# Kernel tuning notes

Measured on AMD Instinct MI355X. Metric: run time of the kernel, lower is better.

## Reference

```python
import jax, jax.numpy as jnp
import numpy as np

VOCAB = 32000
DIM = 1024
SEQ = 4096


def setup_inputs() -> dict:
    key = jax.random.key(0)
    ks = jax.random.split(key, 6)
    x = jax.random.randint(ks[0], (1, SEQ), 0, VOCAB, dtype=jnp.int64 if jax.config.jax_enable_x64 else jnp.int32)
    emb = jax.random.normal(ks[1], (VOCAB, DIM), dtype=jnp.float32) * 0.02
    norm_w = jnp.ones((DIM,), dtype=jnp.float32)
    Wq = jax.random.normal(ks[2], (DIM, DIM), dtype=jnp.float32) * (1.0 / np.sqrt(DIM))
    Wk = jax.random.normal(ks[3], (DIM, DIM), dtype=jnp.float32) * (1.0 / np.sqrt(DIM))
    Wv = jax.random.normal(ks[4], (DIM, DIM), dtype=jnp.float32) * (1.0 / np.sqrt(DIM))
    return {"x": x, "emb": emb, "norm_w": norm_w, "Wq": Wq, "Wk": Wk, "Wv": Wv}


def reference(x, emb, norm_w, Wq, Wk, Wv):
    # embedding lookup: [1, S, D]
    h = emb[x]
    # RMSNorm (torch nn.RMSNorm with eps=None -> finfo(dtype).eps)
    eps = jnp.finfo(h.dtype).eps
    h = h * jax.lax.rsqrt(jnp.mean(h * h, axis=-1, keepdims=True) + eps) * norm_w
    h = h[0]  # squeeze(0) -> [S, D]
    # QKV projections (torch Linear: y = x @ W.T)
    q = h @ Wq.T
    k = h @ Wk.T
    v = h @ Wv.T
    # NOTE: faithful to source -- no 1/sqrt(d) scaling, no causal mask
    attn = jax.nn.softmax(q @ k.T, axis=-1)  # [S, S]
    out = attn @ v  # [S, D]
    return jax.nn.silu(out)
```

## Files before the change

### kernel.cpp

```cpp
#include <hip/hip_runtime.h>
#include <stdint.h>

#define SEQ 4096
#define DIM 1024

typedef __bf16 bf16x8 __attribute__((ext_vector_type(8)));
typedef float f32x4 __attribute__((ext_vector_type(4)));
typedef unsigned short u16;

__device__ __forceinline__ u16 f2bf(float f) {
    unsigned u = __float_as_uint(f);
    u += 0x7fffu + ((u >> 16) & 1u);
    return (u16)(u >> 16);
}
__device__ __forceinline__ float bf2f(u16 h) {
    return __uint_as_float(((unsigned)h) << 16);
}

__device__ __forceinline__ void gload16(const u16* g, u16* l) {
    __builtin_amdgcn_global_load_lds(
        (const __attribute__((address_space(1))) void*)g,
        (__attribute__((address_space(3))) void*)l, 16, 0, 0);
}

__global__ __launch_bounds__(256) void embed_rmsnorm_split(
    const int* __restrict__ x, const float* __restrict__ emb,
    const float* __restrict__ nw, u16* __restrict__ hhl)
{
    const int row  = blockIdx.x;
    const int t    = threadIdx.x;
    const int lane = t & 63, wave = t >> 6;

    bool i64 = true;
    #pragma unroll
    for (int i = 1; i < 128; i += 2) i64 = i64 && (x[i] == 0);
    const int id = i64 ? x[2 * row] : x[row];

    float4 e = *(const float4*)(emb + (size_t)id * DIM + t * 4);
    float ss = e.x*e.x + e.y*e.y + e.z*e.z + e.w*e.w;
    #pragma unroll
    for (int off = 32; off > 0; off >>= 1) ss += __shfl_down(ss, off);

    __shared__ float red[4];
    if (lane == 0) red[wave] = ss;
    __syncthreads();
    float sum = red[0] + red[1] + red[2] + red[3];
    float scale = rsqrtf(sum * (1.0f / DIM) + 1.1920929e-7f);

    float4 n = *(const float4*)(nw + t * 4);
    float o0 = e.x * scale * n.x;
    float o1 = e.y * scale * n.y;
    float o2 = e.z * scale * n.z;
    float o3 = e.w * scale * n.w;
    ushort4 oh, ol;
    u16 b;
    b = f2bf(o0); oh.x = b; ol.x = f2bf(o0 - bf2f(b));
    b = f2bf(o1); oh.y = b; ol.y = f2bf(o1 - bf2f(b));
    b = f2bf(o2); oh.z = b; ol.z = f2bf(o2 - bf2f(b));
    b = f2bf(o3); oh.w = b; ol.w = f2bf(o3 - bf2f(b));
    *(ushort4*)(hhl + (size_t)row * 2048 + t * 4)        = oh;
    *(ushort4*)(hhl + (size_t)row * 2048 + t * 4 + 1024) = ol;
}

__global__ __launch_bounds__(256) void split_w(
    const float* __restrict__ W0, const float* __restrict__ W1,
    const float* __restrict__ W2, u16* __restrict__ Whl)
{
    const float* W = (blockIdx.y == 0) ? W0 : (blockIdx.y == 1) ? W1 : W2;
    const int i   = (blockIdx.x * 256 + threadIdx.x) * 4;
    const int row = i >> 10;
    const int col = i & 1023;
    float4 w = *(const float4*)(W + i);
    ushort4 h, l;
    u16 b;
    b = f2bf(w.x); h.x = b; l.x = f2bf(w.x - bf2f(b));
    b = f2bf(w.y); h.y = b; l.y = f2bf(w.y - bf2f(b));
    b = f2bf(w.z); h.z = b; l.z = f2bf(w.z - bf2f(b));
    b = f2bf(w.w); h.w = b; l.w = f2bf(w.w - bf2f(b));
    u16* d = Whl + (size_t)(blockIdx.y * 1024 + row) * 2048 + col;
    *(ushort4*)(d)        = h;
    *(ushort4*)(d + 1024) = l;
}

#define NT32 32
template<int EPI>
__global__ __launch_bounds__(512, 2) void gemm_bk32(
    const u16* __restrict__ A, const u16* __restrict__ B,
    float* __restrict__ C,
    u16* __restrict__ O0, u16* __restrict__ O1, u16* __restrict__ OT)
{
    __shared__ __align__(16) u16 AhL[2][8192];
    __shared__ __align__(16) u16 AlL[2][8192];
    __shared__ __align__(16) u16 BhL[2][8192];
    __shared__ __align__(16) u16 BlL[2][8192];

    const int tid  = threadIdx.x;
    const int lane = tid & 63;
    const int wid  = tid >> 6;
    const int wm   = wid >> 2;
    const int wn   = wid & 3;
    const int l16  = lane & 15;
    const int half = lane >> 4;

    const int nx  = gridDim.x;
    const int nwg = nx * gridDim.y;
    const int wg  = blockIdx.y * nx + blockIdx.x;
    const int swz = (wg & 7) * (nwg >> 3) + (wg >> 3);
    const int m0  = (swz / nx) * 256;
    const int n0  = (swz % nx) * 256;

    const int srow = tid >> 2;
    const int scol = ((tid & 3) ^ ((tid >> 3) & 3)) * 8;
    const int ldst = tid * 8;
    const u16* pAh[2]; const u16* pAl[2]; const u16* pBh[2]; const u16* pBl[2];
    #pragma unroll
    for (int u = 0; u < 2; ++u) {
        const size_t ao = (size_t)(m0 + u * 128 + srow) * 2048 + scol;
        const size_t bo = (size_t)(n0 + u * 128 + srow) * 2048 + scol;
        pAh[u] = A + ao;  pAl[u] = A + ao + 1024;
        pBh[u] = B + bo;  pBl[u] = B + bo + 1024;
    }

    #pragma unroll
    for (int kk = 0; kk < 2; ++kk)
        #pragma unroll
        for (int u = 0; u < 2; ++u) {
            gload16(pAh[u] + kk * 32, &AhL[kk][u * 4096 + ldst]);
            gload16(pAl[u] + kk * 32, &AlL[kk][u * 4096 + ldst]);
            gload16(pBh[u] + kk * 32, &BhL[kk][u * 4096 + ldst]);
            gload16(pBl[u] + kk * 32, &BlL[kk][u * 4096 + ldst]);
        }
    asm volatile("s_waitcnt vmcnt(8)" ::: "memory");
    __builtin_amdgcn_sched_barrier(0);
    __builtin_amdgcn_s_barrier();

    f32x4 acc[8][4] = {};
    const int rc = 8 * (half ^ ((l16 >> 1) & 3));
    const int ab = (wm * 128 + l16) * 32 + rc;
    const int bb = (wn * 64  + l16) * 32 + rc;

    bf16x8 ah[4], al[4], bh[4], bl[4];

    #pragma unroll 1
    for (int t = 0; t < NT32; ++t) {
        const int  b  = t & 1;
        const bool ds = (t + 2) < NT32;
        const int  k2 = (t + 2) * 32;

        #pragma unroll
        for (int i = 0; i < 4; ++i) {
            ah[i] = *(const bf16x8*)&AhL[b][ab + i * 512];
            al[i] = *(const bf16x8*)&AlL[b][ab + i * 512];
        }
        #pragma unroll
        for (int g = 0; g < 2; ++g) {
            bh[g] = *(const bf16x8*)&BhL[b][bb + g * 512];
            bl[g] = *(const bf16x8*)&BlL[b][bb + g * 512];
        }
        __builtin_amdgcn_s_barrier();
        asm volatile("s_waitcnt lgkmcnt(0)" ::: "memory");
        __builtin_amdgcn_sched_barrier(0);
        __builtin_amdgcn_s_setprio(1);
        #pragma unroll
        for (int i = 0; i < 4; ++i)
            #pragma unroll
            for (int g = 0; g < 2; ++g) {
                acc[i][g] = __builtin_amdgcn_mfma_f32_16x16x32_bf16(ah[i], bh[g], acc[i][g], 0, 0, 0);
                acc[i][g] = __builtin_amdgcn_mfma_f32_16x16x32_bf16(ah[i], bl[g], acc[i][g], 0, 0, 0);
                acc[i][g] = __builtin_amdgcn_mfma_f32_16x16x32_bf16(al[i], bh[g], acc[i][g], 0, 0, 0);
            }
        __builtin_amdgcn_s_setprio(0);
        __builtin_amdgcn_s_barrier();

        #pragma unroll
        for (int g = 0; g < 2; ++g) {
            bh[2 + g] = *(const bf16x8*)&BhL[b][bb + (2 + g) * 512];
            bl[2 + g] = *(const bf16x8*)&BlL[b][bb + (2 + g) * 512];
        }
        __builtin_amdgcn_s_barrier();
        asm volatile("s_waitcnt lgkmcnt(0)" ::: "memory");
        __builtin_amdgcn_sched_barrier(0);
        __builtin_amdgcn_s_setprio(1);
        #pragma unroll
        for (int i = 0; i < 4; ++i)
            #pragma unroll
            for (int g = 0; g < 2; ++g) {
                acc[i][2 + g] = __builtin_amdgcn_mfma_f32_16x16x32_bf16(ah[i], bh[2 + g], acc[i][2 + g], 0, 0, 0);
                acc[i][2 + g] = __builtin_amdgcn_mfma_f32_16x16x32_bf16(ah[i], bl[2 + g], acc[i][2 + g], 0, 0, 0);
                acc[i][2 + g] = __builtin_amdgcn_mfma_f32_16x16x32_bf16(al[i], bh[2 + g], acc[i][2 + g], 0, 0, 0);
            }
        __builtin_amdgcn_s_setprio(0);
        __builtin_amdgcn_s_barrier();

        #pragma unroll
        for (int i = 0; i < 4; ++i) {
            ah[i] = *(const bf16x8*)&AhL[b][ab + 2048 + i * 512];
            al[i] = *(const bf16x8*)&AlL[b][ab + 2048 + i * 512];
        }
        if (ds) {
            gload16(pBh[0] + k2, &BhL[b][ldst]);
            gload16(pBh[1] + k2, &BhL[b][4096 + ldst]);
            gload16(pBl[0] + k2, &BlL[b][ldst]);
            gload16(pBl[1] + k2, &BlL[b][4096 + ldst]);
        }
        __builtin_amdgcn_s_barrier();
        asm volatile("s_waitcnt lgkmcnt(0)" ::: "memory");
        __builtin_amdgcn_sched_barrier(0);
        __builtin_amdgcn_s_setprio(1);
        #pragma unroll
        for (int i = 0; i < 4; ++i)
            #pragma unroll
            for (int g = 0; g < 2; ++g) {
                acc[4 + i][2 + g] = __builtin_amdgcn_mfma_f32_16x16x32_bf16(ah[i], bh[2 + g], acc[4 + i][2 + g], 0, 0, 0);
                acc[4 + i][2 + g] = __builtin_amdgcn_mfma_f32_16x16x32_bf16(ah[i], bl[2 + g], acc[4 + i][2 + g], 0, 0, 0);
                acc[4 + i][2 + g] = __builtin_amdgcn_mfma_f32_16x16x32_bf16(al[i], bh[2 + g], acc[4 + i][2 + g], 0, 0, 0);
            }
        __builtin_amdgcn_s_setprio(0);
        __builtin_amdgcn_s_barrier();

        if (ds) {
            gload16(pAh[0] + k2, &AhL[b][ldst]);
            gload16(pAh[1] + k2, &AhL[b][4096 + ldst]);
            gload16(pAl[0] + k2, &AlL[b][ldst]);
            gload16(pAl[1] + k2, &AlL[b][4096 + ldst]);
        }
        __builtin_amdgcn_s_barrier();
        __builtin_amdgcn_s_setprio(1);
        #pragma unroll
        for (int i = 0; i < 4; ++i)
            #pragma unroll
            for (int g = 0; g < 2; ++g) {
                acc[4 + i][g] = __builtin_amdgcn_mfma_f32_16x16x32_bf16(ah[i], bh[g], acc[4 + i][g], 0, 0, 0);
                acc[4 + i][g] = __builtin_amdgcn_mfma_f32_16x16x32_bf16(ah[i], bl[g], acc[4 + i][g], 0, 0, 0);
                acc[4 + i][g] = __builtin_amdgcn_mfma_f32_16x16x32_bf16(al[i], bh[g], acc[4 + i][g], 0, 0, 0);
            }
        __builtin_amdgcn_s_setprio(0);
        if (t < NT32 - 2) { asm volatile("s_waitcnt vmcnt(8)" ::: "memory"); }
        else              { asm volatile("s_waitcnt vmcnt(0)" ::: "memory"); }
        __builtin_amdgcn_sched_barrier(0);
        __builtin_amdgcn_s_barrier();
    }

    const int crow0 = m0 + wm * 128 + half * 4;
    const int ccol0 = n0 + wn * 64 + l16;
    if constexpr (EPI == 0) {
        #pragma unroll
        for (int mf = 0; mf < 8; ++mf)
            #pragma unroll
            for (int nf = 0; nf < 4; ++nf)
                #pragma unroll
                for (int r = 0; r < 4; ++r)
                    C[(size_t)(crow0 + mf * 16 + r) * SEQ + ccol0 + nf * 16] = acc[mf][nf][r];
    } else {
        const int reg = n0 >> 10;
        #pragma unroll
        for (int mf = 0; mf < 8; ++mf)
            #pragma unroll
            for (int nf = 0; nf < 4; ++nf)
                #pragma unroll
                for (int r = 0; r < 4; ++r) {
                    const int row = crow0 + mf * 16 + r;
                    const int c   = (ccol0 + nf * 16) & 1023;
                    const float val = acc[mf][nf][r];
                    const u16 hi = f2bf(val);
                    if (reg == 0) {
                        O0[(size_t)row * 2048 + c]        = hi;
                        O0[(size_t)row * 2048 + c + 1024] = f2bf(val - bf2f(hi));
                    } else if (reg == 1) {
                        O1[(size_t)row * 2048 + c]        = hi;
                        O1[(size_t)row * 2048 + c + 1024] = f2bf(val - bf2f(hi));
                    } else {
                        OT[(size_t)c * SEQ + row] = hi;
                    }
                }
    }
}

__global__ __launch_bounds__(256) void softmax_rows(float* __restrict__ S)
{
    const int row  = blockIdx.x;
    const int t    = threadIdx.x;
    const int lane = t & 63, wave = t >> 6;
    float* rp = S + (size_t)row * SEQ;

    float v[16];
    #pragma unroll
    for (int i = 0; i < 4; ++i) {
        float4 f = *(const float4*)(rp + i * 1024 + t * 4);
        v[i*4+0] = f.x; v[i*4+1] = f.y; v[i*4+2] = f.z; v[i*4+3] = f.w;
    }

    float m = v[0];
    #pragma unroll
    for (int i = 1; i < 16; ++i) m = fmaxf(m, v[i]);
    #pragma unroll
    for (int off = 32; off > 0; off >>= 1) m = fmaxf(m, __shfl_down(m, off));
    __shared__ float red[4];
    if (lane == 0) red[wave] = m;
    __syncthreads();
    m = fmaxf(fmaxf(red[0], red[1]), fmaxf(red[2], red[3]));
    __syncthreads();

    float s = 0.0f;
    #pragma unroll
    for (int i = 0; i < 16; ++i) { v[i] = __expf(v[i] - m); s += v[i]; }
    #pragma unroll
    for (int off = 32; off > 0; off >>= 1) s += __shfl_down(s, off);
    if (lane == 0) red[wave] = s;
    __syncthreads();
    s = red[0] + red[1] + red[2] + red[3];
    float inv = 1.0f / s;

    u16* op = (u16*)rp;
    #pragma unroll
    for (int i = 0; i < 4; ++i) {
        ushort4 o;
        o.x = f2bf(v[i*4+0] * inv);
        o.y = f2bf(v[i*4+1] * inv);
        o.z = f2bf(v[i*4+2] * inv);
        o.w = f2bf(v[i*4+3] * inv);
        *(ushort4*)(op + i * 1024 + t * 4) = o;
    }
}

__global__ __launch_bounds__(256, 3) void gemm_pv_partial(
    const u16* __restrict__ A, const u16* __restrict__ B,
    float* __restrict__ P0, float* __restrict__ P1)
{
    __shared__ __align__(16) u16 As[128 * 32];
    __shared__ __align__(16) u16 Bs[128 * 32];

    const int tid  = threadIdx.x;
    const int lane = tid & 63;
    const int wave = tid >> 6;
    const int m0   = blockIdx.y * 128;
    const int n0   = blockIdx.x * 128;
    const int wr   = (wave >> 1) * 64;
    const int wc   = (wave & 1) * 64;
    const int half = lane >> 4;
    const int l16  = lane & 15;

    float* C = blockIdx.z ? P1 : P0;
    const int kbase = blockIdx.z * 2048;

    f32x4 acc[4][4] = {};
    const int arow = tid >> 2;
    const int acol = (tid & 3) * 8;
    const int wb   = wave * 512;

    for (int k0 = kbase; k0 < kbase + 2048; k0 += 32) {
        __syncthreads();
        gload16(A + (size_t)(m0 + arow)      * 8192 + k0 + acol, &As[wb]);
        gload16(A + (size_t)(m0 + 64 + arow) * 8192 + k0 + acol, &As[2048 + wb]);
        gload16(B + (size_t)(n0 + arow)      * 4096 + k0 + acol, &Bs[wb]);
        gload16(B + (size_t)(n0 + 64 + arow) * 4096 + k0 + acol, &Bs[2048 + wb]);
        __syncthreads();

        bf16x8 af[4], bfr[4];
        #pragma unroll
        for (int i = 0; i < 4; ++i)
            af[i] = *(const bf16x8*)&As[(wr + i*16 + l16) * 32 + half * 8];
        #pragma unroll
        for (int j = 0; j < 4; ++j)
            bfr[j] = *(const bf16x8*)&Bs[(wc + j*16 + l16) * 32 + half * 8];
        #pragma unroll
        for (int i = 0; i < 4; ++i)
            #pragma unroll
            for (int j = 0; j < 4; ++j)
                acc[i][j] = __builtin_amdgcn_mfma_f32_16x16x32_bf16(af[i], bfr[j], acc[i][j], 0, 0, 0);
    }

    #pragma unroll
    for (int i = 0; i < 4; ++i)
        #pragma unroll
        for (int j = 0; j < 4; ++j)
            #pragma unroll
            for (int r = 0; r < 4; ++r) {
                int row = m0 + wr + i * 16 + half * 4 + r;
                int col = n0 + wc + j * 16 + l16;
                C[(size_t)row * DIM + col] = acc[i][j][r];
            }
}

__global__ __launch_bounds__(256) void combine_silu(
    const float* __restrict__ P0, const float* __restrict__ P1,
    float* __restrict__ out)
{
    const int i = (blockIdx.x * 256 + threadIdx.x) * 4;
    float4 a = *(const float4*)(P0 + i);
    float4 b = *(const float4*)(P1 + i);
    float4 o;
    float v;
    v = a.x + b.x; o.x = v / (1.0f + __expf(-v));
    v = a.y + b.y; o.y = v / (1.0f + __expf(-v));
    v = a.z + b.z; o.z = v / (1.0f + __expf(-v));
    v = a.w + b.w; o.w = v / (1.0f + __expf(-v));
    *(float4*)(out + i) = o;
}

extern "C" void kernel_launch(void* const* d_in, const int* in_sizes, int n_in,
                              void* d_out, int out_size, void* d_ws, size_t ws_size,
                              hipStream_t stream)
{
    const int*   x   = (const int*)d_in[0];
    const float* emb = (const float*)d_in[1];
    const float* nw  = (const float*)d_in[2];
    const float* Wq  = (const float*)d_in[3];
    const float* Wk  = (const float*)d_in[4];
    const float* Wv  = (const float*)d_in[5];
    float* out = (float*)d_out;

    char* ws = (char*)d_ws;
    u16*   vT  = (u16*)(ws);
    u16*   qhl = (u16*)(ws + ( 8u << 20));
    u16*   khl = (u16*)(ws + (24u << 20));
    float* Sc  = (float*)(ws + (40u << 20));
    u16*   hhl = (u16*)(ws + (40u << 20));
    u16*   Whl = (u16*)(ws + (56u << 20));
    float* P0  = (float*)(ws + ( 8u << 20));
    float* P1  = (float*)(ws + (24u << 20));

    embed_rmsnorm_split<<<SEQ, 256, 0, stream>>>(x, emb, nw, hhl);
    split_w<<<dim3(DIM * DIM / 1024, 3), 256, 0, stream>>>(Wq, Wk, Wv, Whl);

    gemm_bk32<1><<<dim3(3072 / 256, SEQ / 256), 512, 0, stream>>>(
        hhl, Whl, nullptr, qhl, khl, vT);

    gemm_bk32<0><<<dim3(SEQ / 256, SEQ / 256), 512, 0, stream>>>(
        qhl, khl, Sc, nullptr, nullptr, nullptr);

    softmax_rows<<<SEQ, 256, 0, stream>>>(Sc);

    gemm_pv_partial<<<dim3(DIM / 128, SEQ / 128, 2), 256, 0, stream>>>(
        (const u16*)Sc, vT, P0, P1);

    combine_silu<<<SEQ * DIM / 1024, 256, 0, stream>>>(P0, P1, out);
}
```

Before: 452.6 us.

## Retile QKV GEMM to 192-wide N tiles and split PV K four ways

The QKV projection GEMM is templated on N-fragment count so it runs with 256x192 tiles (16x16 grid = 256 workgroups) instead of 256x256 (12x16 = 192), aiming for better CU fill. The PV GEMM splits K into four 1024-long chunks instead of two, doubling workgroups. The extra partial sums are written into the unused upper columns of the score buffer, and the combine kernel sums four partials before SiLU. This adds more partial-sum traffic and relies on Sc bf16 data living only in the lower half of each row.

```diff
diff --git a/kernel.cpp b/kernel.cpp
--- a/kernel.cpp
+++ b/kernel.cpp
@@ -83,16 +83,17 @@
 }
 
 #define NT32 32
-template<int EPI>
+template<int EPI, int NF>
 __global__ __launch_bounds__(512, 2) void gemm_bk32(
     const u16* __restrict__ A, const u16* __restrict__ B,
     float* __restrict__ C,
     u16* __restrict__ O0, u16* __restrict__ O1, u16* __restrict__ OT)
 {
+    constexpr int BN = NF * 64;
     __shared__ __align__(16) u16 AhL[2][8192];
     __shared__ __align__(16) u16 AlL[2][8192];
-    __shared__ __align__(16) u16 BhL[2][8192];
-    __shared__ __align__(16) u16 BlL[2][8192];
+    __shared__ __align__(16) u16 BhL[2][NF * 2048];
+    __shared__ __align__(16) u16 BlL[2][NF * 2048];
 
     const int tid  = threadIdx.x;
     const int lane = tid & 63;
@@ -107,39 +108,47 @@
     const int wg  = blockIdx.y * nx + blockIdx.x;
     const int swz = (wg & 7) * (nwg >> 3) + (wg >> 3);
     const int m0  = (swz / nx) * 256;
-    const int n0  = (swz % nx) * 256;
+    const int n0  = (swz % nx) * BN;
 
     const int srow = tid >> 2;
     const int scol = ((tid & 3) ^ ((tid >> 3) & 3)) * 8;
     const int ldst = tid * 8;
-    const u16* pAh[2]; const u16* pAl[2]; const u16* pBh[2]; const u16* pBl[2];
-    #pragma unroll
-    for (int u = 0; u < 2; ++u) {
-        const size_t ao = (size_t)(m0 + u * 128 + srow) * 2048 + scol;
-        const size_t bo = (size_t)(n0 + u * 128 + srow) * 2048 + scol;
-        pAh[u] = A + ao;  pAl[u] = A + ao + 1024;
-        pBh[u] = B + bo;  pBl[u] = B + bo + 1024;
-    }
-
-    #pragma unroll
-    for (int kk = 0; kk < 2; ++kk)
-        #pragma unroll
-        for (int u = 0; u < 2; ++u) {
-            gload16(pAh[u] + kk * 32, &AhL[kk][u * 4096 + ldst]);
-            gload16(pAl[u] + kk * 32, &AlL[kk][u * 4096 + ldst]);
-            gload16(pBh[u] + kk * 32, &BhL[kk][u * 4096 + ldst]);
-            gload16(pBl[u] + kk * 32, &BlL[kk][u * 4096 + ldst]);
-        }
-    asm volatile("s_waitcnt vmcnt(8)" ::: "memory");
+    const u16* pAh0 = A + (size_t)(m0 + srow) * 2048 + scol;
+    const u16* pAh1 = A + (size_t)(m0 + 128 + srow) * 2048 + scol;
+    const u16* pAl0 = pAh0 + 1024;
+    const u16* pAl1 = pAh1 + 1024;
+    const u16* pBh0 = B + (size_t)(n0 + srow) * 2048 + scol;
+    const u16* pBl0 = pBh0 + 1024;
+    const u16* pBh1 = (NF == 4) ? B + (size_t)(n0 + 128 + srow) * 2048 + scol
+                                : B + (size_t)(n0 +  64 + srow) * 2048 + scol;
+    const u16* pBl1 = pBh1 + 1024;
+    const int  bdst1 = (NF == 4) ? 4096 + ldst : 2048 + ldst;
+    const bool doB1  = (NF == 4) || (wid >= 4);
+
+    #pragma unroll
+    for (int kk = 0; kk < 2; ++kk) {
+        gload16(pAh0 + kk * 32, &AhL[kk][ldst]);
+        gload16(pAh1 + kk * 32, &AhL[kk][4096 + ldst]);
+        gload16(pAl0 + kk * 32, &AlL[kk][ldst]);
+        gload16(pAl1 + kk * 32, &AlL[kk][4096 + ldst]);
+        gload16(pBh0 + kk * 32, &BhL[kk][ldst]);
+        gload16(pBl0 + kk * 32, &BlL[kk][ldst]);
+        if (doB1) {
+            gload16(pBh1 + kk * 32, &BhL[kk][bdst1]);
+            gload16(pBl1 + kk * 32, &BlL[kk][bdst1]);
+        }
+    }
+    if (NF == 4 || wid >= 4) { asm volatile("s_waitcnt vmcnt(8)" ::: "memory"); }
+    else                     { asm volatile("s_waitcnt vmcnt(6)" ::: "memory"); }
     __builtin_amdgcn_sched_barrier(0);
     __builtin_amdgcn_s_barrier();
 
-    f32x4 acc[8][4] = {};
+    f32x4 acc[8][NF] = {};
     const int rc = 8 * (half ^ ((l16 >> 1) & 3));
     const int ab = (wm * 128 + l16) * 32 + rc;
-    const int bb = (wn * 64  + l16) * 32 + rc;
-
-    bf16x8 ah[4], al[4], bh[4], bl[4];
+    const int bb = (wn * (NF * 16) + l16) * 32 + rc;
+
+    bf16x8 ah[4], al[4], bh[NF], bl[NF];
 
     #pragma unroll 1
     for (int t = 0; t < NT32; ++t) {
@@ -173,9 +182,9 @@
         __builtin_amdgcn_s_barrier();
 
         #pragma unroll
-        for (int g = 0; g < 2; ++g) {
-            bh[2 + g] = *(const bf16x8*)&BhL[b][bb + (2 + g) * 512];
-            bl[2 + g] = *(const bf16x8*)&BlL[b][bb + (2 + g) * 512];
+        for (int g = 2; g < NF; ++g) {
+            bh[g] = *(const bf16x8*)&BhL[b][bb + g * 512];
+            bl[g] = *(const bf16x8*)&BlL[b][bb + g * 512];
         }
         __builtin_amdgcn_s_barrier();
         asm volatile("s_waitcnt lgkmcnt(0)" ::: "memory");
@@ -184,10 +193,10 @@
         #pragma unroll
         for (int i = 0; i < 4; ++i)
             #pragma unroll
-            for (int g = 0; g < 2; ++g) {
-                acc[i][2 + g] = __builtin_amdgcn_mfma_f32_16x16x32_bf16(ah[i], bh[2 + g], acc[i][2 + g], 0, 0, 0);
-                acc[i][2 + g] = __builtin_amdgcn_mfma_f32_16x16x32_bf16(ah[i], bl[2 + g], acc[i][2 + g], 0, 0, 0);
-                acc[i][2 + g] = __builtin_amdgcn_mfma_f32_16x16x32_bf16(al[i], bh[2 + g], acc[i][2 + g], 0, 0, 0);
+            for (int g = 2; g < NF; ++g) {
+                acc[i][g] = __builtin_amdgcn_mfma_f32_16x16x32_bf16(ah[i], bh[g], acc[i][g], 0, 0, 0);
+                acc[i][g] = __builtin_amdgcn_mfma_f32_16x16x32_bf16(ah[i], bl[g], acc[i][g], 0, 0, 0);
+                acc[i][g] = __builtin_amdgcn_mfma_f32_16x16x32_bf16(al[i], bh[g], acc[i][g], 0, 0, 0);
             }
         __builtin_amdgcn_s_setprio(0);
         __builtin_amdgcn_s_barrier();
@@ -198,10 +207,12 @@
             al[i] = *(const bf16x8*)&AlL[b][ab + 2048 + i * 512];
         }
         if (ds) {
-            gload16(pBh[0] + k2, &BhL[b][ldst]);
-            gload16(pBh[1] + k2, &BhL[b][4096 + ldst]);
-            gload16(pBl[0] + k2, &BlL[b][ldst]);
-            gload16(pBl[1] + k2, &BlL[b][4096 + ldst]);
+            gload16(pBh0 + k2, &BhL[b][ldst]);
+            gload16(pBl0 + k2, &BlL[b][ldst]);
+            if (doB1) {
+                gload16(pBh1 + k2, &BhL[b][bdst1]);
+                gload16(pBl1 + k2, &BlL[b][bdst1]);
+            }
         }
         __builtin_amdgcn_s_barrier();
         asm volatile("s_waitcnt lgkmcnt(0)" ::: "memory");
@@ -210,19 +221,19 @@
         #pragma unroll
         for (int i = 0; i < 4; ++i)
             #pragma unroll
-            for (int g = 0; g < 2; ++g) {
-                acc[4 + i][2 + g] = __builtin_amdgcn_mfma_f32_16x16x32_bf16(ah[i], bh[2 + g], acc[4 + i][2 + g], 0, 0, 0);
-                acc[4 + i][2 + g] = __builtin_amdgcn_mfma_f32_16x16x32_bf16(ah[i], bl[2 + g], acc[4 + i][2 + g], 0, 0, 0);
-                acc[4 + i][2 + g] = __builtin_amdgcn_mfma_f32_16x16x32_bf16(al[i], bh[2 + g], acc[4 + i][2 + g], 0, 0, 0);
+            for (int g = 2; g < NF; ++g) {
+                acc[4 + i][g] = __builtin_amdgcn_mfma_f32_16x16x32_bf16(ah[i], bh[g], acc[4 + i][g], 0, 0, 0);
+                acc[4 + i][g] = __builtin_amdgcn_mfma_f32_16x16x32_bf16(ah[i], bl[g], acc[4 + i][g], 0, 0, 0);
+                acc[4 + i][g] = __builtin_amdgcn_mfma_f32_16x16x32_bf16(al[i], bh[g], acc[4 + i][g], 0, 0, 0);
             }
         __builtin_amdgcn_s_setprio(0);
         __builtin_amdgcn_s_barrier();
 
         if (ds) {
-            gload16(pAh[0] + k2, &AhL[b][ldst]);
-            gload16(pAh[1] + k2, &AhL[b][4096 + ldst]);
-            gload16(pAl[0] + k2, &AlL[b][ldst]);
-            gload16(pAl[1] + k2, &AlL[b][4096 + ldst]);
+            gload16(pAh0 + k2, &AhL[b][ldst]);
+            gload16(pAh1 + k2, &AhL[b][4096 + ldst]);
+            gload16(pAl0 + k2, &AlL[b][ldst]);
+            gload16(pAl1 + k2, &AlL[b][4096 + ldst]);
         }
         __builtin_amdgcn_s_barrier();
         __builtin_amdgcn_s_setprio(1);
@@ -235,32 +246,37 @@
                 acc[4 + i][g] = __builtin_amdgcn_mfma_f32_16x16x32_bf16(al[i], bh[g], acc[4 + i][g], 0, 0, 0);
             }
         __builtin_amdgcn_s_setprio(0);
-        if (t < NT32 - 2) { asm volatile("s_waitcnt vmcnt(8)" ::: "memory"); }
-        else              { asm volatile("s_waitcnt vmcnt(0)" ::: "memory"); }
+        if (t < NT32 - 2) {
+            if (NF == 4 || wid >= 4) { asm volatile("s_waitcnt vmcnt(8)" ::: "memory"); }
+            else                     { asm volatile("s_waitcnt vmcnt(6)" ::: "memory"); }
+        } else {
+            asm volatile("s_waitcnt vmcnt(0)" ::: "memory");
+        }
         __builtin_amdgcn_sched_barrier(0);
         __builtin_amdgcn_s_barrier();
     }
 
     const int crow0 = m0 + wm * 128 + half * 4;
-    const int ccol0 = n0 + wn * 64 + l16;
+    const int wcol  = n0 + wn * (NF * 16);
     if constexpr (EPI == 0) {
         #pragma unroll
         for (int mf = 0; mf < 8; ++mf)
             #pragma unroll
-            for (int nf = 0; nf < 4; ++nf)
+            for (int nf = 0; nf < NF; ++nf)
                 #pragma unroll
                 for (int r = 0; r < 4; ++r)
-                    C[(size_t)(crow0 + mf * 16 + r) * SEQ + ccol0 + nf * 16] = acc[mf][nf][r];
+                    C[(size_t)(crow0 + mf * 16 + r) * SEQ + wcol + nf * 16 + l16] = acc[mf][nf][r];
     } else {
-        const int reg = n0 >> 10;
-        #pragma unroll
-        for (int mf = 0; mf < 8; ++mf)
-            #pragma unroll
-            for (int nf = 0; nf < 4; ++nf)
+        #pragma unroll
+        for (int nf = 0; nf < NF; ++nf) {
+            const int base = wcol + nf * 16;
+            const int reg  = base >> 10;
+            const int c    = (base & 1023) + l16;
+            #pragma unroll
+            for (int mf = 0; mf < 8; ++mf)
                 #pragma unroll
                 for (int r = 0; r < 4; ++r) {
                     const int row = crow0 + mf * 16 + r;
-                    const int c   = (ccol0 + nf * 16) & 1023;
                     const float val = acc[mf][nf][r];
                     const u16 hi = f2bf(val);
                     if (reg == 0) {
@@ -273,6 +289,7 @@
                         OT[(size_t)c * SEQ + row] = hi;
                     }
                 }
+        }
     }
 }
 
@@ -325,7 +342,7 @@
 
 __global__ __launch_bounds__(256, 3) void gemm_pv_partial(
     const u16* __restrict__ A, const u16* __restrict__ B,
-    float* __restrict__ P0, float* __restrict__ P1)
+    float* __restrict__ P0, float* __restrict__ P1, float* __restrict__ Sg)
 {
     __shared__ __align__(16) u16 As[128 * 32];
     __shared__ __align__(16) u16 Bs[128 * 32];
@@ -340,15 +357,20 @@
     const int half = lane >> 4;
     const int l16  = lane & 15;
 
-    float* C = blockIdx.z ? P1 : P0;
-    const int kbase = blockIdx.z * 2048;
+    const int z = blockIdx.z;
+    float* C;
+    int ldc2;
+    if      (z == 0) { C = P0;                      ldc2 = 1024; }
+    else if (z == 1) { C = P1;                      ldc2 = 1024; }
+    else             { C = Sg + 2048 + (z - 2) * 1024; ldc2 = 4096; }
+    const int kbase = z * 1024;
 
     f32x4 acc[4][4] = {};
     const int arow = tid >> 2;
     const int acol = (tid & 3) * 8;
     const int wb   = wave * 512;
 
-    for (int k0 = kbase; k0 < kbase + 2048; k0 += 32) {
+    for (int k0 = kbase; k0 < kbase + 1024; k0 += 32) {
         __syncthreads();
         gload16(A + (size_t)(m0 + arow)      * 8192 + k0 + acol, &As[wb]);
         gload16(A + (size_t)(m0 + 64 + arow) * 8192 + k0 + acol, &As[2048 + wb]);
@@ -378,23 +400,28 @@
             for (int r = 0; r < 4; ++r) {
                 int row = m0 + wr + i * 16 + half * 4 + r;
                 int col = n0 + wc + j * 16 + l16;
-                C[(size_t)row * DIM + col] = acc[i][j][r];
-            }
-}
-
-__global__ __launch_bounds__(256) void combine_silu(
+                C[(size_t)row * ldc2 + col] = acc[i][j][r];
+            }
+}
+
+__global__ __launch_bounds__(256) void combine_silu4(
     const float* __restrict__ P0, const float* __restrict__ P1,
-    float* __restrict__ out)
+    const float* __restrict__ Sg, float* __restrict__ out)
 {
     const int i = (blockIdx.x * 256 + threadIdx.x) * 4;
+    const int r = i >> 10;
+    const int c = i & 1023;
+    const float* g = Sg + (size_t)r * 4096 + 2048 + c;
     float4 a = *(const float4*)(P0 + i);
     float4 b = *(const float4*)(P1 + i);
+    float4 d = *(const float4*)(g);
+    float4 e = *(const float4*)(g + 1024);
     float4 o;
     float v;
-    v = a.x + b.x; o.x = v / (1.0f + __expf(-v));
-    v = a.y + b.y; o.y = v / (1.0f + __expf(-v));
-    v = a.z + b.z; o.z = v / (1.0f + __expf(-v));
-    v = a.w + b.w; o.w = v / (1.0f + __expf(-v));
+    v = a.x + b.x + d.x + e.x; o.x = v / (1.0f + __expf(-v));
+    v = a.y + b.y + d.y + e.y; o.y = v / (1.0f + __expf(-v));
+    v = a.z + b.z + d.z + e.z; o.z = v / (1.0f + __expf(-v));
+    v = a.w + b.w + d.w + e.w; o.w = v / (1.0f + __expf(-v));
     *(float4*)(out + i) = o;
 }
 
@@ -423,16 +450,16 @@
     embed_rmsnorm_split<<<SEQ, 256, 0, stream>>>(x, emb, nw, hhl);
     split_w<<<dim3(DIM * DIM / 1024, 3), 256, 0, stream>>>(Wq, Wk, Wv, Whl);
 
-    gemm_bk32<1><<<dim3(3072 / 256, SEQ / 256), 512, 0, stream>>>(
+    gemm_bk32<1, 3><<<dim3(3072 / 192, SEQ / 256), 512, 0, stream>>>(
         hhl, Whl, nullptr, qhl, khl, vT);
 
-    gemm_bk32<0><<<dim3(SEQ / 256, SEQ / 256), 512, 0, stream>>>(
+    gemm_bk32<0, 4><<<dim3(SEQ / 256, SEQ / 256), 512, 0, stream>>>(
         qhl, khl, Sc, nullptr, nullptr, nullptr);
 
     softmax_rows<<<SEQ, 256, 0, stream>>>(Sc);
 
-    gemm_pv_partial<<<dim3(DIM / 128, SEQ / 128, 2), 256, 0, stream>>>(
-        (const u16*)Sc, vT, P0, P1);
-
-    combine_silu<<<SEQ * DIM / 1024, 256, 0, stream>>>(P0, P1, out);
-}
+    gemm_pv_partial<<<dim3(DIM / 128, SEQ / 128, 4), 256, 0, stream>>>(
+        (const u16*)Sc, vT, P0, P1, Sc);
+
+    combine_silu4<<<SEQ * DIM / 1024, 256, 0, stream>>>(P0, P1, Sc, out);
+}
```

Measured after the change: 471.2 us. +4.1%, slower.
